# Performance work log

Measured on AMD Instinct MI355X. Metric: run time of the kernel, lower is better.

Reference implementation:

```python
import jax, jax.numpy as jnp
import numpy as np

N_NODES = 25000
N_EDGES = 100000
N_GRAPHS = 1000
DIM = 64
NUM_FEAT = 14
EDGE_FEAT = 4
HIDDEN_EDGE = 128
NUM_OUT = 1
NUM_CONV_STEPS = 3
SET2SET_STEPS = 3
NEG_SLOPE = 0.01


def leaky_relu(x):
    return jnp.where(x > 0, x, NEG_SLOPE * x)


def setup_inputs() -> dict:
    key = jax.random.key(0)
    ks = jax.random.split(key, 24)
    s = lambda fan_in: 1.0 / np.sqrt(fan_in)
    inp = {
        "x": jax.random.normal(ks[0], (N_NODES, NUM_FEAT), dtype=jnp.float32),
        "edge_index": jax.random.randint(ks[1], (2, N_EDGES), 0, N_NODES),
        "edge_attr": jax.random.uniform(ks[2], (N_EDGES, EDGE_FEAT), dtype=jnp.float32),
        "batch": jnp.sort(jax.random.randint(ks[3], (N_NODES,), 0, N_GRAPHS)),
        # lin0
        "lin0_w": jax.random.normal(ks[4], (DIM, NUM_FEAT), dtype=jnp.float32) * s(NUM_FEAT),
        "lin0_b": jnp.zeros((DIM,), dtype=jnp.float32),
        # edge-weight MLP: Linear(4,128) -> LeakyReLU -> Linear(128, DIM*DIM)
        "net_w1": jax.random.normal(ks[5], (HIDDEN_EDGE, EDGE_FEAT), dtype=jnp.float32) * s(EDGE_FEAT),
        "net_b1": jnp.zeros((HIDDEN_EDGE,), dtype=jnp.float32),
        "net_w2": jax.random.normal(ks[6], (DIM * DIM, HIDDEN_EDGE), dtype=jnp.float32) * s(HIDDEN_EDGE),
        "net_b2": jnp.zeros((DIM * DIM,), dtype=jnp.float32),
        # NNConv root weight + bias
        "conv_root": jax.random.normal(ks[7], (DIM, DIM), dtype=jnp.float32) * s(DIM),
        "conv_bias": jnp.zeros((DIM,), dtype=jnp.float32),
        # GRU (single layer), torch gate order r,z,n
        "gru_w_ih": jax.random.normal(ks[8], (3 * DIM, DIM), dtype=jnp.float32) * s(DIM),
        "gru_w_hh": jax.random.normal(ks[9], (3 * DIM, DIM), dtype=jnp.float32) * s(DIM),
        "gru_b_ih": jnp.zeros((3 * DIM,), dtype=jnp.float32),
        "gru_b_hh": jnp.zeros((3 * DIM,), dtype=jnp.float32),
        # Set2Set LSTM: input 2*DIM -> hidden DIM, torch gate order i,f,g,o
        "lstm_w_ih": jax.random.normal(ks[10], (4 * DIM, 2 * DIM), dtype=jnp.float32) * s(2 * DIM),
        "lstm_w_hh": jax.random.normal(ks[11], (4 * DIM, DIM), dtype=jnp.float32) * s(DIM),
        "lstm_b_ih": jnp.zeros((4 * DIM,), dtype=jnp.float32),
        "lstm_b_hh": jnp.zeros((4 * DIM,), dtype=jnp.float32),
        # final linear on [B, 2*DIM]
        "lin_w": jax.random.normal(ks[12], (NUM_OUT, 2 * DIM), dtype=jnp.float32) * s(2 * DIM),
        "lin_b": jnp.zeros((NUM_OUT,), dtype=jnp.float32),
    }
    return inp


def _forward(x, edge_index, edge_attr, batch,
             lin0_w, lin0_b, net_w1, net_b1, net_w2, net_b2,
             conv_root, conv_bias, gru_w_ih, gru_w_hh, gru_b_ih, gru_b_hh,
             lstm_w_ih, lstm_w_hh, lstm_b_ih, lstm_b_hh, lin_w, lin_b):
    src, dst = edge_index[0], edge_index[1]

    out = leaky_relu(x @ lin0_w.T + lin0_b)          # [N, DIM]
    h = out                                          # GRU hidden [N, DIM]

    # edge_attr is constant across conv steps -> dynamic weights computed once
    W_e = (leaky_relu(edge_attr @ net_w1.T + net_b1) @ net_w2.T + net_b2)
    W_e = W_e.reshape(N_EDGES, DIM, DIM)             # [E, DIM, DIM]

    deg = jax.ops.segment_sum(jnp.ones((N_EDGES,), dtype=x.dtype), dst,
                              num_segments=N_NODES)
    inv_deg = jnp.where(deg > 0, 1.0 / jnp.maximum(deg, 1.0), 0.0)[:, None]

    for _ in range(NUM_CONV_STEPS):
        # NNConv: gather -> per-edge matmul -> scatter-mean, plus root term
        msg = jnp.einsum('ed,edo->eo', out[src], W_e)                 # [E, DIM]
        aggr = jax.ops.segment_sum(msg, dst, num_segments=N_NODES) * inv_deg
        m = leaky_relu(aggr + out @ conv_root + conv_bias)
        # single-step GRU (torch equations, gate order r,z,n)
        gi = m @ gru_w_ih.T + gru_b_ih
        gh = h @ gru_w_hh.T + gru_b_hh
        i_r, i_z, i_n = jnp.split(gi, 3, axis=-1)
        h_r, h_z, h_n = jnp.split(gh, 3, axis=-1)
        r = jax.nn.sigmoid(i_r + h_r)
        z = jax.nn.sigmoid(i_z + h_z)
        n = jnp.tanh(i_n + r * h_n)
        h = (1.0 - z) * n + z * h
        out = h

    # Set2Set pooling (processing_steps=3)
    q_star = jnp.zeros((N_GRAPHS, 2 * DIM), dtype=x.dtype)
    hl = jnp.zeros((N_GRAPHS, DIM), dtype=x.dtype)
    cl = jnp.zeros((N_GRAPHS, DIM), dtype=x.dtype)
    for _ in range(SET2SET_STEPS):
        gates = q_star @ lstm_w_ih.T + lstm_b_ih + hl @ lstm_w_hh.T + lstm_b_hh
        gi, gf, gg, go = jnp.split(gates, 4, axis=-1)
        cl = jax.nn.sigmoid(gf) * cl + jax.nn.sigmoid(gi) * jnp.tanh(gg)
        hl = jax.nn.sigmoid(go) * jnp.tanh(cl)
        q = hl                                                         # [B, DIM]
        e = jnp.sum(out * q[batch], axis=-1)                           # [N]
        e_max = jax.ops.segment_max(e, batch, num_segments=N_GRAPHS)
        e_exp = jnp.exp(e - e_max[batch])
        denom = jax.ops.segment_sum(e_exp, batch, num_segments=N_GRAPHS)
        a = e_exp / denom[batch]                                       # segment softmax
        r_read = jax.ops.segment_sum(a[:, None] * out, batch,
                                     num_segments=N_GRAPHS)            # [B, DIM]
        q_star = jnp.concatenate([q, r_read], axis=-1)

    return q_star @ lin_w.T + lin_b                                    # [B, NUM_OUT]


def reference(x, edge_index, edge_attr, batch,
              lin0_w, lin0_b, net_w1, net_b1, net_w2, net_b2,
              conv_root, conv_bias, gru_w_ih, gru_w_hh, gru_b_ih, gru_b_hh,
              lstm_w_ih, lstm_w_hh, lstm_b_ih, lstm_b_hh, lin_w, lin_b):
    return _forward(x, edge_index, edge_attr, batch,
                    lin0_w, lin0_b, net_w1, net_b1, net_w2, net_b2,
                    conv_root, conv_bias, gru_w_ih, gru_w_hh, gru_b_ih, gru_b_hh,
                    lstm_w_ih, lstm_w_hh, lstm_b_ih, lstm_b_hh, lin_w, lin_b)
```

## Files before the change

kernel.cpp:

```cpp
#include <hip/hip_runtime.h>
#include <math.h>

#define N_NODES_C  25000
#define N_EDGES_C  100000
#define N_GRAPHS_C 1000
#define EPB 128

typedef __attribute__((ext_vector_type(8))) _Float16 f16x8;
typedef __attribute__((ext_vector_type(2))) _Float16 f16x2;
typedef __attribute__((ext_vector_type(4))) float   f32x4;

__device__ __forceinline__ float lrelu(float x) { return x > 0.f ? x : 0.01f * x; }
__device__ __forceinline__ float sigm(float x)  { return 1.f / (1.f + __expf(-x)); }
__device__ __forceinline__ f32x4 MFH(f16x8 a, f16x8 b, f32x4 c) {
  return __builtin_amdgcn_mfma_f32_16x16x32_f16(a, b, c, 0, 0, 0);
}

__global__ __launch_bounds__(256) void lin0_kernel(const float* __restrict__ x,
                            const float* __restrict__ w, const float* __restrict__ b,
                            float* __restrict__ nodeF) {
  __shared__ float ws[64 * 15];
  __shared__ float bs[64];
  __shared__ float xr[4][16];
  const int tid = threadIdx.x;
  for (int i = tid; i < 896; i += 256) { int o = i / 14, j = i % 14; ws[o * 15 + j] = w[i]; }
  if (tid < 64) bs[tid] = b[tid];
  const int nl = tid >> 6, o = tid & 63;
  const int n = blockIdx.x * 4 + nl;
  if (o < 14 && n < N_NODES_C) xr[nl][o] = x[n * 14 + o];
  __syncthreads();
  if (n < N_NODES_C) {
    float s = bs[o];
#pragma unroll
    for (int j = 0; j < 14; ++j) s += xr[nl][j] * ws[o * 15 + j];
    nodeF[n * 64 + o] = lrelu(s);
  }
}

__global__ void deg_kernel(const int* __restrict__ ei, float* __restrict__ deg) {
  int e = blockIdx.x * blockDim.x + threadIdx.x;
  if (e < N_EDGES_C) atomicAdd(&deg[ei[N_EDGES_C + e]], 1.f);
}

__global__ void invdeg_kernel(float* __restrict__ deg) {
  int n = blockIdx.x * blockDim.x + threadIdx.x;
  if (n < N_NODES_C) { float v = deg[n]; deg[n] = v > 0.f ? 1.f / v : 0.f; }
}

__global__ void goff_kernel(const int* __restrict__ batch, int* __restrict__ goff) {
  int g = blockIdx.x * blockDim.x + threadIdx.x;
  if (g > N_GRAPHS_C) return;
  int lo = 0, hi = N_NODES_C;
  while (lo < hi) { int mid = (lo + hi) >> 1; if (batch[mid] < g) lo = mid + 1; else hi = mid; }
  goff[g] = lo;
}

__global__ void prep_gru_kernel(const float* __restrict__ conv_root,
                                const float* __restrict__ w_ih, const float* __restrict__ w_hh,
                                _Float16* __restrict__ Rtp,
                                _Float16* __restrict__ Wip, _Float16* __restrict__ Whp) {
  int i = blockIdx.x * 256 + threadIdx.x;
  if (i < 12288) {
    int j = i & 7, lane = (i >> 3) & 63, kc = (i >> 9) & 1, t = i >> 10;
    int o = t * 16 + (lane & 15), d = kc * 32 + (lane >> 4) * 8 + j;
    if (i < 4096) Rtp[i] = (_Float16)conv_root[d * 64 + o];
    Wip[i] = (_Float16)w_ih[o * 64 + d];
    Whp[i] = (_Float16)w_hh[o * 64 + d];
  }
}

__global__ __launch_bounds__(256) void prep_w2_kernel(
    const float* __restrict__ net_w2, const float* __restrict__ net_b2,
    _Float16* __restrict__ Wp, _Float16* __restrict__ B2p) {
  int i = blockIdx.x * 256 + threadIdx.x;
  {
    int j = i & 7, lane = (i >> 3) & 63, q = (i >> 9) & 3, p = (i >> 11) & 1;
    int oh = (i >> 12) & 1, d = i >> 13;
    int kci = q >> 1, ob = q & 1;
    int col = lane & 15, kg = lane >> 4;
    int o = oh * 32 + ob * 16 + col, h = (p * 2 + kci) * 32 + kg * 8 + j;
    Wp[i] = (_Float16)net_w2[((size_t)d * 64 + o) * 128 + h];
  }
  if (i < 4096) {
    int j = i & 7, lane = (i >> 3) & 63, kc2 = (i >> 9) & 1, ob = (i >> 10) & 1, oh = (i >> 11) & 1;
    int col = lane & 15, kg = lane >> 4;
    int o = oh * 32 + ob * 16 + col, d = kc2 * 32 + kg * 8 + j;
    B2p[i] = (_Float16)net_b2[d * 64 + o];
  }
}

__global__ __launch_bounds__(256, 3) void msg_kernel(
    const float* __restrict__ nodef,
    const int*   __restrict__ ei,
    const float* __restrict__ eattr,
    const float* __restrict__ net_w1,
    const float* __restrict__ net_b1,
    const _Float16* __restrict__ Wp,
    const _Float16* __restrict__ B2p,
    float* __restrict__ aggr)
{
  __shared__ _Float16 xsT[EPB * 64];
  __shared__ float    w1s[128 * 5];

  const int tid = threadIdx.x;
  const int e0 = blockIdx.x * EPB;

  if (tid < 128) {
    float4 wv = *(const float4*)(net_w1 + tid * 4);
    w1s[tid * 5 + 0] = wv.x; w1s[tid * 5 + 1] = wv.y;
    w1s[tid * 5 + 2] = wv.z; w1s[tid * 5 + 3] = wv.w;
    w1s[tid * 5 + 4] = net_b1[tid];
  }
  {
    const int e = tid >> 1, dh = (tid & 1) * 32;
    int ge = e0 + e;
    const int esw = (e & 7) << 3;
#pragma unroll
    for (int jb = 0; jb < 4; ++jb) {
      int d = dh + jb * 8;
      float4 v0, v1;
      if (ge < N_EDGES_C) {
        const float4* nf4 = (const float4*)(nodef + (size_t)ei[ge] * 64 + d);
        v0 = nf4[0]; v1 = nf4[1];
      } else {
        v0 = make_float4(0.f, 0.f, 0.f, 0.f); v1 = v0;
      }
      f16x8 pk;
      pk[0] = (_Float16)v0.x; pk[1] = (_Float16)v0.y; pk[2] = (_Float16)v0.z; pk[3] = (_Float16)v0.w;
      pk[4] = (_Float16)v1.x; pk[5] = (_Float16)v1.y; pk[6] = (_Float16)v1.z; pk[7] = (_Float16)v1.w;
      *(f16x8*)&xsT[e * 64 + (d ^ esw)] = pk;
    }
  }

  const int lane = tid & 63, wv = tid >> 6;
  const int e0w = (wv & 1) * 64;
  const int oh  = wv >> 1;
  const int col = lane & 15;
  const int kg  = lane >> 4;
  const int swz = (col & 7) << 3;

  __syncthreads();

  f32x4 acc[4][2];
#pragma unroll
  for (int eb = 0; eb < 4; ++eb) { acc[eb][0] = 0.f; acc[eb][1] = 0.f; }
#pragma unroll
  for (int ob = 0; ob < 2; ++ob)
#pragma unroll
    for (int kc2 = 0; kc2 < 2; ++kc2) {
      f16x8 b2f = *(const f16x8*)(B2p + oh * 2048 + ob * 1024 + kc2 * 512 + lane * 8);
#pragma unroll
      for (int eb = 0; eb < 4; ++eb) {
        f16x8 xf = *(const f16x8*)&xsT[(e0w + eb * 16 + col) * 64 + ((kc2 * 32 + kg * 8) ^ swz)];
        acc[eb][ob] = MFH(xf, b2f, acc[eb][ob]);
      }
    }

#define ISSUE(BUF, ADDR)                                                  \
  asm volatile("global_load_dwordx4 %0, %4, off\n\t"                      \
               "global_load_dwordx4 %1, %4, off offset:1024\n\t"          \
               "global_load_dwordx4 %2, %4, off offset:2048\n\t"          \
               "global_load_dwordx4 %3, %4, off offset:3072"              \
               : "=&v"(BUF[0]), "=&v"(BUF[1]), "=&v"(BUF[2]), "=&v"(BUF[3]) \
               : "v"(ADDR)                                                \
               : "memory")
#define COMPUTE(BUF, XV, J)                                               \
  {                                                                       \
    _Pragma("unroll")                                                     \
    for (int eb = 0; eb < 4; ++eb) {                                      \
      unsigned dw = XV[eb].u[(J) >> 1];                                   \
      unsigned xd = __builtin_amdgcn_perm(dw, dw, ((J) & 1) ? 0x03020302u : 0x01000100u); \
      f16x2 x2; { union { unsigned u; f16x2 h; } c; c.u = xd; x2 = c.h; } \
      _Pragma("unroll")                                                   \
      for (int kci = 0; kci < 2; ++kci) {                                 \
        union { f16x8 v; f16x2 pp[4]; } af, Uu;                           \
        af.v = Af[eb][kci];                                               \
        _Pragma("unroll")                                                 \
        for (int q = 0; q < 4; ++q) Uu.pp[q] = af.pp[q] * x2;             \
        acc[eb][0] = MFH(Uu.v, BUF[kci * 2 + 0], acc[eb][0]);             \
        acc[eb][1] = MFH(Uu.v, BUF[kci * 2 + 1], acc[eb][1]);             \
      }                                                                   \
    }                                                                     \
  }

  const _Float16* wp_base = Wp + oh * 4096 + lane * 8;
#pragma unroll 1
  for (int p = 0; p < 2; ++p) {
    f16x8 Af[4][2];
    {
      float4 at[4];
#pragma unroll
      for (int eb = 0; eb < 4; ++eb) {
        int ge = e0 + e0w + eb * 16 + col;
        at[eb] = (ge < N_EDGES_C) ? *(const float4*)(eattr + (size_t)ge * 4)
                                  : make_float4(0.f, 0.f, 0.f, 0.f);
      }
#pragma unroll
      for (int kci = 0; kci < 2; ++kci) {
        float4 wr[8]; float wb[8];
#pragma unroll
        for (int j = 0; j < 8; ++j) {
          int hq = (p * 2 + kci) * 32 + kg * 8 + j;
          wr[j] = *(const float4*)&w1s[hq * 5];
          wb[j] = w1s[hq * 5 + 4];
        }
#pragma unroll
        for (int eb = 0; eb < 4; ++eb) {
          f16x8 F;
#pragma unroll
          for (int j = 0; j < 8; ++j) {
            float a = wb[j] + at[eb].x * wr[j].x + at[eb].y * wr[j].y
                            + at[eb].z * wr[j].z + at[eb].w * wr[j].w;
            F[j] = (_Float16)lrelu(a);
          }
          Af[eb][kci] = F;
        }
      }
    }

    const _Float16* wp_p = wp_base + p * 2048;
    f16x8 B0[4], B1[4];
    ISSUE(B0, wp_p);
    ISSUE(B1, wp_p + 8192);

#pragma unroll 1
    for (int d8 = 0; d8 < 64; d8 += 8) {
      union XU { f16x8 v; unsigned u[4]; };
      XU XV[4];
#pragma unroll
      for (int eb = 0; eb < 4; ++eb)
        XV[eb].v = *(const f16x8*)&xsT[(e0w + eb * 16 + col) * 64 + (d8 ^ swz)];
#pragma unroll
      for (int j = 0; j < 8; ++j) {
        const int d = d8 + j;
        if (d < 63) { asm volatile("s_waitcnt vmcnt(4)"); }
        else        { asm volatile("s_waitcnt vmcnt(0)"); }
        __builtin_amdgcn_sched_barrier(0);
        if ((j & 1) == 0) { COMPUTE(B0, XV, j); } else { COMPUTE(B1, XV, j); }
        __builtin_amdgcn_sched_barrier(0);
        if (d < 62) {
          const _Float16* adr = wp_p + (size_t)(d + 2) * 8192;
          if ((j & 1) == 0) { ISSUE(B0, adr); } else { ISSUE(B1, adr); }
        }
      }
    }
  }
#undef ISSUE
#undef COMPUTE

  const int o0w = oh * 32;
#pragma unroll
  for (int eb = 0; eb < 4; ++eb) {
#pragma unroll
    for (int r = 0; r < 4; ++r) {
      int e = e0w + eb * 16 + kg * 4 + r;
      int ge = e0 + e;
      if (ge < N_EDGES_C) {
        int dn = ei[N_EDGES_C + ge];
        atomicAdd(&aggr[(size_t)dn * 64 + o0w + col],      acc[eb][0][r]);
        atomicAdd(&aggr[(size_t)dn * 64 + o0w + 16 + col], acc[eb][1][r]);
      }
    }
  }
}

__global__ __launch_bounds__(256) void node_update_kernel(
    float* __restrict__ aggr, const float* __restrict__ invdeg,
    const _Float16* __restrict__ Rtp, const _Float16* __restrict__ Wip,
    const _Float16* __restrict__ Whp,
    const float* __restrict__ conv_bias,
    const float* __restrict__ b_ih, const float* __restrict__ b_hh,
    float* __restrict__ nodeF)
{
  __shared__ _Float16 ms[4][16 * 64];

  const int tid = threadIdx.x, lane = tid & 63, wv = tid >> 6;
  const int col = lane & 15, kg = lane >> 4;
  const int nwb = blockIdx.x * 64 + wv * 16;

  int arow = nwb + col; if (arow >= N_NODES_C) arow = N_NODES_C - 1;
  f16x8 nf[2];
#pragma unroll
  for (int kc = 0; kc < 2; ++kc) {
    f32x4 v0 = *(const f32x4*)(nodeF + (size_t)arow * 64 + kc * 32 + kg * 8);
    f32x4 v1 = *(const f32x4*)(nodeF + (size_t)arow * 64 + kc * 32 + kg * 8 + 4);
    f16x8 F;
#pragma unroll
    for (int j = 0; j < 4; ++j) { F[j] = (_Float16)v0[j]; F[4 + j] = (_Float16)v1[j]; }
    nf[kc] = F;
  }

  f32x4 racc[4];
#pragma unroll
  for (int t = 0; t < 4; ++t) racc[t] = conv_bias[t * 16 + col];
#pragma unroll
  for (int t = 0; t < 4; ++t)
#pragma unroll
    for (int kc = 0; kc < 2; ++kc)
      racc[t] = MFH(nf[kc], *(const f16x8*)(Rtp + t * 1024 + kc * 512 + lane * 8), racc[t]);

  float invd[4]; int nrow[4];
#pragma unroll
  for (int r = 0; r < 4; ++r) {
    int nn = nwb + kg * 4 + r; nrow[r] = nn;
    invd[r] = (nn < N_NODES_C) ? invdeg[nn] : 0.f;
  }
#pragma unroll
  for (int t = 0; t < 4; ++t) {
#pragma unroll
    for (int r = 0; r < 4; ++r) {
      int nn = nrow[r];
      float ag = 0.f;
      if (nn < N_NODES_C) {
        size_t idx = (size_t)nn * 64 + t * 16 + col;
        ag = aggr[idx];
        aggr[idx] = 0.f;
      }
      float mval = lrelu(ag * invd[r] + racc[t][r]);
      int nl = kg * 4 + r;
      int dsw = (t * 16 + col) ^ ((nl & 7) << 3);
      ms[wv][nl * 64 + dsw] = (_Float16)mval;
    }
  }
  __syncthreads();

  f16x8 ma[2];
#pragma unroll
  for (int kc = 0; kc < 2; ++kc)
    ma[kc] = *(const f16x8*)&ms[wv][col * 64 + ((kc * 32 + kg * 8) ^ ((col & 7) << 3))];

  f32x4 gi[12], gh[12];
#pragma unroll
  for (int t = 0; t < 12; ++t) { gi[t] = b_ih[t * 16 + col]; gh[t] = b_hh[t * 16 + col]; }
#pragma unroll
  for (int t = 0; t < 12; ++t)
#pragma unroll
    for (int kc = 0; kc < 2; ++kc) {
      gi[t] = MFH(ma[kc], *(const f16x8*)(Wip + t * 1024 + kc * 512 + lane * 8), gi[t]);
      gh[t] = MFH(nf[kc], *(const f16x8*)(Whp + t * 1024 + kc * 512 + lane * 8), gh[t]);
    }

#pragma unroll
  for (int t = 0; t < 4; ++t) {
#pragma unroll
    for (int r = 0; r < 4; ++r) {
      int nn = nrow[r];
      if (nn >= N_NODES_C) continue;
      size_t idx = (size_t)nn * 64 + t * 16 + col;
      float hv = nodeF[idx];
      float rr = sigm(gi[t][r] + gh[t][r]);
      float zz = sigm(gi[t + 4][r] + gh[t + 4][r]);
      float nv = tanhf(gi[t + 8][r] + rr * gh[t + 8][r]);
      nodeF[idx] = (1.f - zz) * nv + zz * hv;
    }
  }
}

__global__ __launch_bounds__(64) void set2set_kernel(
    const float* __restrict__ nodeF, const int* __restrict__ goff,
    const float* __restrict__ w_ih, const float* __restrict__ w_hh,
    const float* __restrict__ b_ih, const float* __restrict__ b_hh,
    const float* __restrict__ lw, const float* __restrict__ lb,
    float* __restrict__ ebuf, float* __restrict__ dout)
{
  const int g = blockIdx.x, t = threadIdx.x;
  __shared__ float qs[128], hs[64];
  float hl = 0.f, cl = 0.f;
  qs[t] = 0.f; qs[64 + t] = 0.f;
  const int s0 = goff[g], s1 = goff[g + 1];

  for (int step = 0; step < 3; ++step) {
    hs[t] = hl;
    __syncthreads();
    float gv[4];
#pragma unroll
    for (int k = 0; k < 4; ++k) {
      float s = b_ih[k * 64 + t] + b_hh[k * 64 + t];
      const float4* wi4 = (const float4*)(w_ih + (k * 64 + t) * 128);
#pragma unroll 8
      for (int j = 0; j < 32; ++j) {
        float4 w = wi4[j];
        s += qs[4 * j] * w.x + qs[4 * j + 1] * w.y + qs[4 * j + 2] * w.z + qs[4 * j + 3] * w.w;
      }
      const float4* wh4 = (const float4*)(w_hh + (k * 64 + t) * 64);
#pragma unroll 8
      for (int j = 0; j < 16; ++j) {
        float4 w = wh4[j];
        s += hs[4 * j] * w.x + hs[4 * j + 1] * w.y + hs[4 * j + 2] * w.z + hs[4 * j + 3] * w.w;
      }
      gv[k] = s;
    }
    cl = sigm(gv[1]) * cl + sigm(gv[0]) * tanhf(gv[2]);
    hl = sigm(gv[3]) * tanhf(cl);
    const float qv = hl;

    float emax = -3.0e38f;
    for (int n = s0; n < s1; ++n) {
      float p = nodeF[n * 64 + t] * qv;
#pragma unroll
      for (int off = 32; off > 0; off >>= 1) p += __shfl_down(p, off);
      float en = __shfl(p, 0);
      if (t == 0) ebuf[n] = en;
      emax = fmaxf(emax, en);
    }
    __syncthreads();
    float lsum = 0.f;
    for (int n = s0 + t; n < s1; n += 64) {
      float ex = __expf(ebuf[n] - emax);
      ebuf[n] = ex;
      lsum += ex;
    }
#pragma unroll
    for (int off = 32; off > 0; off >>= 1) lsum += __shfl_down(lsum, off);
    float denom = __shfl(lsum, 0);
    __syncthreads();
    float r = 0.f;
    for (int n = s0; n < s1; ++n) r += ebuf[n] * nodeF[n * 64 + t];
    if (s1 > s0) r /= denom;
    qs[t] = qv; qs[64 + t] = r;
  }
  __syncthreads();
  float s = qs[t] * lw[t] + qs[64 + t] * lw[64 + t];
#pragma unroll
  for (int off = 32; off > 0; off >>= 1) s += __shfl_down(s, off);
  if (t == 0) dout[g] = s + lb[0];
}

extern "C" void kernel_launch(void* const* d_in, const int* in_sizes, int n_in,
                              void* d_out, int out_size, void* d_ws, size_t ws_size,
                              hipStream_t stream) {
  const float* x         = (const float*)d_in[0];
  const int*   ei        = (const int*)  d_in[1];
  const float* eattr     = (const float*)d_in[2];
  const int*   batch     = (const int*)  d_in[3];
  const float* lin0_w    = (const float*)d_in[4];
  const float* lin0_b    = (const float*)d_in[5];
  const float* net_w1    = (const float*)d_in[6];
  const float* net_b1    = (const float*)d_in[7];
  const float* net_w2    = (const float*)d_in[8];
  const float* net_b2    = (const float*)d_in[9];
  const float* conv_root = (const float*)d_in[10];
  const float* conv_bias = (const float*)d_in[11];
  const float* gru_w_ih  = (const float*)d_in[12];
  const float* gru_w_hh  = (const float*)d_in[13];
  const float* gru_b_ih  = (const float*)d_in[14];
  const float* gru_b_hh  = (const float*)d_in[15];
  const float* lstm_w_ih = (const float*)d_in[16];
  const float* lstm_w_hh = (const float*)d_in[17];
  const float* lstm_b_ih = (const float*)d_in[18];
  const float* lstm_b_hh = (const float*)d_in[19];
  const float* lin_w     = (const float*)d_in[20];
  const float* lin_b     = (const float*)d_in[21];

  float* ws    = (float*)d_ws;
  float* nodeF = ws;
  float* aggr  = nodeF + 1600000;
  float* deg   = aggr + 1600000;
  float* ebuf  = deg + 25000;
  int*   goff  = (int*)(ebuf + 25000);
  _Float16* Rtp = (_Float16*)(goff + 1024);
  _Float16* Wip = Rtp + 4096;
  _Float16* Whp = Wip + 12288;
  _Float16* Wp  = Whp + 12288;
  _Float16* B2p = Wp + 524288;

  hipMemsetAsync(deg, 0, 25000 * sizeof(float), stream);
  hipMemsetAsync(aggr, 0, 1600000 * sizeof(float), stream);

  lin0_kernel<<<(N_NODES_C + 3) / 4, 256, 0, stream>>>(x, lin0_w, lin0_b, nodeF);
  deg_kernel<<<(N_EDGES_C + 255) / 256, 256, 0, stream>>>(ei, deg);
  invdeg_kernel<<<(N_NODES_C + 255) / 256, 256, 0, stream>>>(deg);
  goff_kernel<<<(N_GRAPHS_C + 256) / 256, 256, 0, stream>>>(batch, goff);
  prep_gru_kernel<<<48, 256, 0, stream>>>(conv_root, gru_w_ih, gru_w_hh, Rtp, Wip, Whp);
  prep_w2_kernel<<<2048, 256, 0, stream>>>(net_w2, net_b2, Wp, B2p);

  for (int step = 0; step < 3; ++step) {
    msg_kernel<<<(N_EDGES_C + EPB - 1) / EPB, 256, 0, stream>>>(
        nodeF, ei, eattr, net_w1, net_b1, Wp, B2p, aggr);
    node_update_kernel<<<(N_NODES_C + 63) / 64, 256, 0, stream>>>(
        aggr, deg, Rtp, Wip, Whp, conv_bias, gru_b_ih, gru_b_hh, nodeF);
  }

  set2set_kernel<<<N_GRAPHS_C, 64, 0, stream>>>(
      nodeF, goff, lstm_w_ih, lstm_w_hh, lstm_b_ih, lstm_b_hh, lin_w, lin_b, ebuf, (float*)d_out);
}
```

Before: 587.9 us.

## Merge setup kernels, hoist loads, shrink node-update blocks, parallelize set2set

Folds the goff binary search into deg_kernel and the GRU weight packing into the w2 prep kernel, removing two launches. In msg_kernel the edge-attribute loads move out of the p loop so they are issued once. node_update_kernel now uses 128-thread blocks covering 32 nodes and issues its aggr/invdeg loads before the root-weight MFMAs. set2set uses 256 threads per graph, splitting the LSTM gates and the per-node attention loops across four wavefronts with shared-memory reductions. The cost is more barriers and more reduction overhead in set2set.

Result: faster. 564.6 us (median of 2 runs) (-4.0%).

```diff
diff --git a/kernel.cpp b/kernel.cpp
--- a/kernel.cpp
+++ b/kernel.cpp
@@ -37,9 +37,15 @@
   }
 }
 
-__global__ void deg_kernel(const int* __restrict__ ei, float* __restrict__ deg) {
+__global__ void deg_kernel(const int* __restrict__ ei, const int* __restrict__ batch,
+                           float* __restrict__ deg, int* __restrict__ goff) {
   int e = blockIdx.x * blockDim.x + threadIdx.x;
   if (e < N_EDGES_C) atomicAdd(&deg[ei[N_EDGES_C + e]], 1.f);
+  if (e <= N_GRAPHS_C) {
+    int lo = 0, hi = N_NODES_C;
+    while (lo < hi) { int mid = (lo + hi) >> 1; if (batch[mid] < e) lo = mid + 1; else hi = mid; }
+    goff[e] = lo;
+  }
 }
 
 __global__ void invdeg_kernel(float* __restrict__ deg) {
@@ -47,31 +53,12 @@
   if (n < N_NODES_C) { float v = deg[n]; deg[n] = v > 0.f ? 1.f / v : 0.f; }
 }
 
-__global__ void goff_kernel(const int* __restrict__ batch, int* __restrict__ goff) {
-  int g = blockIdx.x * blockDim.x + threadIdx.x;
-  if (g > N_GRAPHS_C) return;
-  int lo = 0, hi = N_NODES_C;
-  while (lo < hi) { int mid = (lo + hi) >> 1; if (batch[mid] < g) lo = mid + 1; else hi = mid; }
-  goff[g] = lo;
-}
-
-__global__ void prep_gru_kernel(const float* __restrict__ conv_root,
-                                const float* __restrict__ w_ih, const float* __restrict__ w_hh,
-                                _Float16* __restrict__ Rtp,
-                                _Float16* __restrict__ Wip, _Float16* __restrict__ Whp) {
-  int i = blockIdx.x * 256 + threadIdx.x;
-  if (i < 12288) {
-    int j = i & 7, lane = (i >> 3) & 63, kc = (i >> 9) & 1, t = i >> 10;
-    int o = t * 16 + (lane & 15), d = kc * 32 + (lane >> 4) * 8 + j;
-    if (i < 4096) Rtp[i] = (_Float16)conv_root[d * 64 + o];
-    Wip[i] = (_Float16)w_ih[o * 64 + d];
-    Whp[i] = (_Float16)w_hh[o * 64 + d];
-  }
-}
-
-__global__ __launch_bounds__(256) void prep_w2_kernel(
+__global__ __launch_bounds__(256) void prep_kernel(
     const float* __restrict__ net_w2, const float* __restrict__ net_b2,
-    _Float16* __restrict__ Wp, _Float16* __restrict__ B2p) {
+    const float* __restrict__ conv_root,
+    const float* __restrict__ w_ih, const float* __restrict__ w_hh,
+    _Float16* __restrict__ Wp, _Float16* __restrict__ B2p,
+    _Float16* __restrict__ Rtp, _Float16* __restrict__ Wip, _Float16* __restrict__ Whp) {
   int i = blockIdx.x * 256 + threadIdx.x;
   {
     int j = i & 7, lane = (i >> 3) & 63, q = (i >> 9) & 3, p = (i >> 11) & 1;
@@ -86,6 +73,13 @@
     int col = lane & 15, kg = lane >> 4;
     int o = oh * 32 + ob * 16 + col, d = kc2 * 32 + kg * 8 + j;
     B2p[i] = (_Float16)net_b2[d * 64 + o];
+  }
+  if (i < 12288) {
+    int j = i & 7, lane = (i >> 3) & 63, kc = (i >> 9) & 1, t = i >> 10;
+    int o = t * 16 + (lane & 15), d = kc * 32 + (lane >> 4) * 8 + j;
+    if (i < 4096) Rtp[i] = (_Float16)conv_root[d * 64 + o];
+    Wip[i] = (_Float16)w_ih[o * 64 + d];
+    Whp[i] = (_Float16)w_hh[o * 64 + d];
   }
 }
 
@@ -155,6 +149,14 @@
         acc[eb][ob] = MFH(xf, b2f, acc[eb][ob]);
       }
     }
+
+  float4 at[4];
+#pragma unroll
+  for (int eb = 0; eb < 4; ++eb) {
+    int ge = e0 + e0w + eb * 16 + col;
+    at[eb] = (ge < N_EDGES_C) ? *(const float4*)(eattr + (size_t)ge * 4)
+                              : make_float4(0.f, 0.f, 0.f, 0.f);
+  }
 
 #define ISSUE(BUF, ADDR)                                                  \
   asm volatile("global_load_dwordx4 %0, %4, off\n\t"                      \
@@ -187,34 +189,25 @@
 #pragma unroll 1
   for (int p = 0; p < 2; ++p) {
     f16x8 Af[4][2];
-    {
-      float4 at[4];
+#pragma unroll
+    for (int kci = 0; kci < 2; ++kci) {
+      float4 wr[8]; float wb[8];
+#pragma unroll
+      for (int j = 0; j < 8; ++j) {
+        int hq = (p * 2 + kci) * 32 + kg * 8 + j;
+        wr[j] = *(const float4*)&w1s[hq * 5];
+        wb[j] = w1s[hq * 5 + 4];
+      }
 #pragma unroll
       for (int eb = 0; eb < 4; ++eb) {
-        int ge = e0 + e0w + eb * 16 + col;
-        at[eb] = (ge < N_EDGES_C) ? *(const float4*)(eattr + (size_t)ge * 4)
-                                  : make_float4(0.f, 0.f, 0.f, 0.f);
-      }
-#pragma unroll
-      for (int kci = 0; kci < 2; ++kci) {
-        float4 wr[8]; float wb[8];
+        f16x8 F;
 #pragma unroll
         for (int j = 0; j < 8; ++j) {
-          int hq = (p * 2 + kci) * 32 + kg * 8 + j;
-          wr[j] = *(const float4*)&w1s[hq * 5];
-          wb[j] = w1s[hq * 5 + 4];
+          float a = wb[j] + at[eb].x * wr[j].x + at[eb].y * wr[j].y
+                          + at[eb].z * wr[j].z + at[eb].w * wr[j].w;
+          F[j] = (_Float16)lrelu(a);
         }
-#pragma unroll
-        for (int eb = 0; eb < 4; ++eb) {
-          f16x8 F;
-#pragma unroll
-          for (int j = 0; j < 8; ++j) {
-            float a = wb[j] + at[eb].x * wr[j].x + at[eb].y * wr[j].y
-                            + at[eb].z * wr[j].z + at[eb].w * wr[j].w;
-            F[j] = (_Float16)lrelu(a);
-          }
-          Af[eb][kci] = F;
-        }
+        Af[eb][kci] = F;
       }
     }
 
@@ -264,7 +257,7 @@
   }
 }
 
-__global__ __launch_bounds__(256) void node_update_kernel(
+__global__ __launch_bounds__(128) void node_update_kernel(
     float* __restrict__ aggr, const float* __restrict__ invdeg,
     const _Float16* __restrict__ Rtp, const _Float16* __restrict__ Wip,
     const _Float16* __restrict__ Whp,
@@ -272,11 +265,26 @@
     const float* __restrict__ b_ih, const float* __restrict__ b_hh,
     float* __restrict__ nodeF)
 {
-  __shared__ _Float16 ms[4][16 * 64];
+  __shared__ _Float16 ms[2][16 * 64];
 
   const int tid = threadIdx.x, lane = tid & 63, wv = tid >> 6;
   const int col = lane & 15, kg = lane >> 4;
-  const int nwb = blockIdx.x * 64 + wv * 16;
+  const int nwb = blockIdx.x * 32 + wv * 16;
+
+  float invd[4]; int nrow[4];
+#pragma unroll
+  for (int r = 0; r < 4; ++r) {
+    int nn = nwb + kg * 4 + r; nrow[r] = nn;
+    invd[r] = (nn < N_NODES_C) ? invdeg[nn] : 0.f;
+  }
+  float ag[4][4];
+#pragma unroll
+  for (int t = 0; t < 4; ++t)
+#pragma unroll
+    for (int r = 0; r < 4; ++r) {
+      int nn = nrow[r];
+      ag[t][r] = (nn < N_NODES_C) ? aggr[(size_t)nn * 64 + t * 16 + col] : 0.f;
+    }
 
   int arow = nwb + col; if (arow >= N_NODES_C) arow = N_NODES_C - 1;
   f16x8 nf[2];
@@ -299,24 +307,13 @@
     for (int kc = 0; kc < 2; ++kc)
       racc[t] = MFH(nf[kc], *(const f16x8*)(Rtp + t * 1024 + kc * 512 + lane * 8), racc[t]);
 
-  float invd[4]; int nrow[4];
-#pragma unroll
-  for (int r = 0; r < 4; ++r) {
-    int nn = nwb + kg * 4 + r; nrow[r] = nn;
-    invd[r] = (nn < N_NODES_C) ? invdeg[nn] : 0.f;
-  }
 #pragma unroll
   for (int t = 0; t < 4; ++t) {
 #pragma unroll
     for (int r = 0; r < 4; ++r) {
       int nn = nrow[r];
-      float ag = 0.f;
-      if (nn < N_NODES_C) {
-        size_t idx = (size_t)nn * 64 + t * 16 + col;
-        ag = aggr[idx];
-        aggr[idx] = 0.f;
-      }
-      float mval = lrelu(ag * invd[r] + racc[t][r]);
+      if (nn < N_NODES_C) aggr[(size_t)nn * 64 + t * 16 + col] = 0.f;
+      float mval = lrelu(ag[t][r] * invd[r] + racc[t][r]);
       int nl = kg * 4 + r;
       int dsw = (t * 16 + col) ^ ((nl & 7) << 3);
       ms[wv][nl * 64 + dsw] = (_Float16)mval;
@@ -356,74 +353,88 @@
   }
 }
 
-__global__ __launch_bounds__(64) void set2set_kernel(
+__global__ __launch_bounds__(256) void set2set_kernel(
     const float* __restrict__ nodeF, const int* __restrict__ goff,
     const float* __restrict__ w_ih, const float* __restrict__ w_hh,
     const float* __restrict__ b_ih, const float* __restrict__ b_hh,
     const float* __restrict__ lw, const float* __restrict__ lb,
     float* __restrict__ ebuf, float* __restrict__ dout)
 {
-  const int g = blockIdx.x, t = threadIdx.x;
-  __shared__ float qs[128], hs[64];
-  float hl = 0.f, cl = 0.f;
-  qs[t] = 0.f; qs[64 + t] = 0.f;
+  const int g = blockIdx.x, tid = threadIdx.x;
+  const int t = tid & 63, grp = tid >> 6;
+  __shared__ float qs[128], hs[64], cls[64], gvs[4][64], red[4][64], scal[8];
+  if (tid < 128) qs[tid] = 0.f;
+  if (tid < 64) { hs[tid] = 0.f; cls[tid] = 0.f; }
   const int s0 = goff[g], s1 = goff[g + 1];
+  __syncthreads();
 
   for (int step = 0; step < 3; ++step) {
-    hs[t] = hl;
-    __syncthreads();
-    float gv[4];
-#pragma unroll
-    for (int k = 0; k < 4; ++k) {
-      float s = b_ih[k * 64 + t] + b_hh[k * 64 + t];
-      const float4* wi4 = (const float4*)(w_ih + (k * 64 + t) * 128);
+    {
+      float s = b_ih[grp * 64 + t] + b_hh[grp * 64 + t];
+      const float4* wi4 = (const float4*)(w_ih + (grp * 64 + t) * 128);
 #pragma unroll 8
       for (int j = 0; j < 32; ++j) {
         float4 w = wi4[j];
         s += qs[4 * j] * w.x + qs[4 * j + 1] * w.y + qs[4 * j + 2] * w.z + qs[4 * j + 3] * w.w;
       }
-      const float4* wh4 = (const float4*)(w_hh + (k * 64 + t) * 64);
+      const float4* wh4 = (const float4*)(w_hh + (grp * 64 + t) * 64);
 #pragma unroll 8
       for (int j = 0; j < 16; ++j) {
         float4 w = wh4[j];
         s += hs[4 * j] * w.x + hs[4 * j + 1] * w.y + hs[4 * j + 2] * w.z + hs[4 * j + 3] * w.w;
       }
-      gv[k] = s;
-    }
-    cl = sigm(gv[1]) * cl + sigm(gv[0]) * tanhf(gv[2]);
-    hl = sigm(gv[3]) * tanhf(cl);
-    const float qv = hl;
+      gvs[grp][t] = s;
+    }
+    __syncthreads();
+    if (tid < 64) {
+      float c = sigm(gvs[1][t]) * cls[t] + sigm(gvs[0][t]) * tanhf(gvs[2][t]);
+      float hn = sigm(gvs[3][t]) * tanhf(c);
+      cls[t] = c; hs[t] = hn; qs[t] = hn;
+    }
+    __syncthreads();
+    const float qv = hs[t];
 
     float emax = -3.0e38f;
-    for (int n = s0; n < s1; ++n) {
-      float p = nodeF[n * 64 + t] * qv;
+    for (int n = s0 + grp; n < s1; n += 4) {
+      float p = nodeF[(size_t)n * 64 + t] * qv;
 #pragma unroll
       for (int off = 32; off > 0; off >>= 1) p += __shfl_down(p, off);
       float en = __shfl(p, 0);
       if (t == 0) ebuf[n] = en;
       emax = fmaxf(emax, en);
     }
-    __syncthreads();
+    if (t == 0) scal[grp] = emax;
+    __syncthreads();
+    emax = fmaxf(fmaxf(scal[0], scal[1]), fmaxf(scal[2], scal[3]));
+
     float lsum = 0.f;
-    for (int n = s0 + t; n < s1; n += 64) {
+    for (int n = s0 + tid; n < s1; n += 256) {
       float ex = __expf(ebuf[n] - emax);
       ebuf[n] = ex;
       lsum += ex;
     }
 #pragma unroll
     for (int off = 32; off > 0; off >>= 1) lsum += __shfl_down(lsum, off);
-    float denom = __shfl(lsum, 0);
-    __syncthreads();
+    if (t == 0) scal[4 + grp] = lsum;
+    __syncthreads();
+    float denom = scal[4] + scal[5] + scal[6] + scal[7];
+
     float r = 0.f;
-    for (int n = s0; n < s1; ++n) r += ebuf[n] * nodeF[n * 64 + t];
-    if (s1 > s0) r /= denom;
-    qs[t] = qv; qs[64 + t] = r;
-  }
+    for (int n = s0 + grp; n < s1; n += 4) r += ebuf[n] * nodeF[(size_t)n * 64 + t];
+    red[grp][t] = r;
+    __syncthreads();
+    if (tid < 64) {
+      float rr = red[0][t] + red[1][t] + red[2][t] + red[3][t];
+      qs[64 + t] = (s1 > s0) ? rr / denom : 0.f;
+    }
+    __syncthreads();
+  }
+  float sacc = (tid < 128) ? qs[tid] * lw[tid] : 0.f;
+#pragma unroll
+  for (int off = 32; off > 0; off >>= 1) sacc += __shfl_down(sacc, off);
+  if (t == 0) scal[grp] = sacc;
   __syncthreads();
-  float s = qs[t] * lw[t] + qs[64 + t] * lw[64 + t];
-#pragma unroll
-  for (int off = 32; off > 0; off >>= 1) s += __shfl_down(s, off);
-  if (t == 0) dout[g] = s + lb[0];
+  if (tid == 0) dout[g] = scal[0] + scal[1] + lb[0];
 }
 
 extern "C" void kernel_launch(void* const* d_in, const int* in_sizes, int n_in,
@@ -468,19 +479,18 @@
   hipMemsetAsync(aggr, 0, 1600000 * sizeof(float), stream);
 
   lin0_kernel<<<(N_NODES_C + 3) / 4, 256, 0, stream>>>(x, lin0_w, lin0_b, nodeF);
-  deg_kernel<<<(N_EDGES_C + 255) / 256, 256, 0, stream>>>(ei, deg);
+  deg_kernel<<<(N_EDGES_C + 255) / 256, 256, 0, stream>>>(ei, batch, deg, goff);
   invdeg_kernel<<<(N_NODES_C + 255) / 256, 256, 0, stream>>>(deg);
-  goff_kernel<<<(N_GRAPHS_C + 256) / 256, 256, 0, stream>>>(batch, goff);
-  prep_gru_kernel<<<48, 256, 0, stream>>>(conv_root, gru_w_ih, gru_w_hh, Rtp, Wip, Whp);
-  prep_w2_kernel<<<2048, 256, 0, stream>>>(net_w2, net_b2, Wp, B2p);
+  prep_kernel<<<2048, 256, 0, stream>>>(net_w2, net_b2, conv_root, gru_w_ih, gru_w_hh,
+                                        Wp, B2p, Rtp, Wip, Whp);
 
   for (int step = 0; step < 3; ++step) {
     msg_kernel<<<(N_EDGES_C + EPB - 1) / EPB, 256, 0, stream>>>(
         nodeF, ei, eattr, net_w1, net_b1, Wp, B2p, aggr);
-    node_update_kernel<<<(N_NODES_C + 63) / 64, 256, 0, stream>>>(
+    node_update_kernel<<<(N_NODES_C + 31) / 32, 128, 0, stream>>>(
         aggr, deg, Rtp, Wip, Whp, conv_bias, gru_b_ih, gru_b_hh, nodeF);
   }
 
-  set2set_kernel<<<N_GRAPHS_C, 64, 0, stream>>>(
+  set2set_kernel<<<N_GRAPHS_C, 256, 0, stream>>>(
       nodeF, goff, lstm_w_ih, lstm_w_hh, lstm_b_ih, lstm_b_hh, lin_w, lin_b, ebuf, (float*)d_out);
 }
```
